# Kernel tuning notes

Measured on AMD Instinct MI355X. Metric: run time of the kernel, lower is better.

## Reference

```python
import jax, jax.numpy as jnp
import numpy as np

N = 100000      # nodes
E = 1600000     # edges (before self loops)
G = 64          # graphs (drones)
H = 4           # heads
C = 64          # hidden_channels (per-head dim, concat=False)
NODE_F = 32
DRONE_F = 16
OUT = 32
L = 2           # num_layers
LN_EPS = 1e-5
NEG_SLOPE = 0.2


def setup_inputs() -> dict:
    key = jax.random.key(0)
    ks = jax.random.split(key, 20)
    gn = lambda k, shape, s=0.1: jax.random.normal(k, shape, jnp.float32) * s
    inp = {}
    inp["x"] = jax.random.normal(ks[0], (N, NODE_F), jnp.float32)
    inp["drone_feat"] = jax.random.normal(ks[1], (G, DRONE_F), jnp.float32)
    inp["edge_index"] = jax.random.randint(ks[2], (2, E), 0, N, jnp.int32)
    inp["batch"] = jnp.sort(jax.random.randint(ks[3], (N,), 0, G, jnp.int32))
    inp["node_W"] = gn(ks[4], (C, NODE_F)); inp["node_b"] = jnp.zeros((C,), jnp.float32)
    inp["drone_W"] = gn(ks[5], (C, DRONE_F)); inp["drone_b"] = jnp.zeros((C,), jnp.float32)
    for l in range(L):
        kk = jax.random.split(ks[6 + l], 3)
        inp[f"convW{l}"] = gn(kk[0], (H * C, C))
        inp[f"att_src{l}"] = gn(kk[1], (H, C))
        inp[f"att_dst{l}"] = gn(kk[2], (H, C))
        inp[f"convb{l}"] = jnp.zeros((C,), jnp.float32)
        inp[f"ln_g{l}"] = jnp.ones((C,), jnp.float32)
        inp[f"ln_b{l}"] = jnp.zeros((C,), jnp.float32)
    inp["out_W"] = gn(ks[10], (OUT, C)); inp["out_b"] = jnp.zeros((OUT,), jnp.float32)
    return inp


def _layer_norm(x, g, b):
    mu = jnp.mean(x, axis=-1, keepdims=True)
    var = jnp.mean((x - mu) ** 2, axis=-1, keepdims=True)
    return (x - mu) * jax.lax.rsqrt(var + LN_EPS) * g + b


def _gat_conv(h, src, dst, W, a_src, a_dst, b):
    # h: [N, C] -> per-head transform [N, H, C]
    xh = (h @ W.T).reshape(N, H, C)
    alpha_s = jnp.sum(xh * a_src[None], axis=-1)  # [N, H]
    alpha_d = jnp.sum(xh * a_dst[None], axis=-1)  # [N, H]
    e = jax.nn.leaky_relu(alpha_s[src] + alpha_d[dst], NEG_SLOPE)  # [E', H]
    m = jax.ops.segment_max(e, dst, num_segments=N)  # segment softmax over dst
    ex = jnp.exp(e - m[dst])
    s = jax.ops.segment_sum(ex, dst, num_segments=N)
    alpha = ex / (s[dst] + 1e-16)                   # [E', H]
    out = jax.ops.segment_sum(xh[src] * alpha[:, :, None], dst, num_segments=N)
    return jnp.mean(out, axis=1) + b                # concat=False -> head mean


def reference(x, edge_index, drone_feat, batch, node_W, node_b, drone_W, drone_b,
              convW0, att_src0, att_dst0, convb0, ln_g0, ln_b0,
              convW1, att_src1, att_dst1, convb1, ln_g1, ln_b1,
              out_W, out_b):
    # add self loops (PyG GATConv default add_self_loops=True)
    loop = jnp.arange(N, dtype=edge_index.dtype)
    src = jnp.concatenate([edge_index[0], loop])
    dst = jnp.concatenate([edge_index[1], loop])
    h = x @ node_W.T + node_b + (drone_feat @ drone_W.T + drone_b)[batch]
    layers = [(convW0, att_src0, att_dst0, convb0, ln_g0, ln_b0),
              (convW1, att_src1, att_dst1, convb1, ln_g1, ln_b1)]
    for (W, a_s, a_d, cb, g, lb) in layers:
        h = h + jax.nn.relu(_layer_norm(_gat_conv(h, src, dst, W, a_s, a_d, cb), g, lb))
    return h @ out_W.T + out_b
```

## Files before the change

### kernel.cpp

```cpp
#include <hip/hip_runtime.h>
#include <hip/hip_fp16.h>
#include <math.h>


#define NEG_SLOPE 0.2f
#define LN_EPS 1e-5f

struct __align__(8) h16x4 { __half x, y, z, w; };

__global__ __launch_bounds__(256) void k_h0(
        const float* __restrict__ x, const int* __restrict__ batch,
        const float* __restrict__ node_W, const float* __restrict__ drone_W,
        const float* __restrict__ node_b, const float* __restrict__ drone_b,
        const float* __restrict__ drone_feat,
        float* __restrict__ h, int* __restrict__ cnt, int N) {
    __shared__ float xs[16][33];
    __shared__ float ds[16][17];
    __shared__ float wn[32][65];
    __shared__ float wd[16][65];
    __shared__ float bs[64];
    int t = threadIdx.x;
    int n0 = blockIdx.x * 16;
    for (int i = t; i < 2048; i += 256) { int co = i >> 5, k = i & 31; wn[k][co] = node_W[i]; }
    for (int i = t; i < 1024; i += 256) { int co = i >> 4, k = i & 15; wd[k][co] = drone_W[i]; }
    if (t < 64) bs[t] = node_b[t] + drone_b[t];
    for (int i = t; i < 512; i += 256) {
        int r = i >> 5, c = i & 31;
        int n = n0 + r;
        xs[r][c] = (n < N) ? x[(size_t)n * 32 + c] : 0.f;
    }
    {
        int r = t >> 4, c = t & 15;
        int n = n0 + r;
        int g = (n < N) ? batch[n] : 0;
        ds[r][c] = drone_feat[g * 16 + c];
    }
    {
        int gt = blockIdx.x * 256 + t;
        if (gt < N) cnt[gt] = 0;
    }
    __syncthreads();
    int co = t & 63;
    int nsub = t >> 6;
    float b = bs[co];
    float a0 = b, a1 = b, a2 = b, a3 = b;
#pragma unroll
    for (int k = 0; k < 32; ++k) {
        float w = wn[k][co];
        a0 = fmaf(xs[nsub * 4 + 0][k], w, a0);
        a1 = fmaf(xs[nsub * 4 + 1][k], w, a1);
        a2 = fmaf(xs[nsub * 4 + 2][k], w, a2);
        a3 = fmaf(xs[nsub * 4 + 3][k], w, a3);
    }
#pragma unroll
    for (int k = 0; k < 16; ++k) {
        float w = wd[k][co];
        a0 = fmaf(ds[nsub * 4 + 0][k], w, a0);
        a1 = fmaf(ds[nsub * 4 + 1][k], w, a1);
        a2 = fmaf(ds[nsub * 4 + 2][k], w, a2);
        a3 = fmaf(ds[nsub * 4 + 3][k], w, a3);
    }
    float av[4] = {a0, a1, a2, a3};
#pragma unroll
    for (int j = 0; j < 4; ++j) {
        int n = n0 + nsub * 4 + j;
        if (n < N) h[(size_t)n * 64 + co] = av[j];
    }
}

__global__ void k_scatter(const int* __restrict__ edge_index, int* __restrict__ cnt,
                          int* __restrict__ csrB,
                          const float* __restrict__ cW0, const float* __restrict__ cW1,
                          const float* __restrict__ s0, const float* __restrict__ d0,
                          const float* __restrict__ s1, const float* __restrict__ d1,
                          const float* __restrict__ out_W,
                          float* __restrict__ wt0, float* __restrict__ wt1,
                          float* __restrict__ uv, float* __restrict__ owT,
                          int E, int S) {
    if (blockIdx.y == 0 && blockIdx.x < 128) {
        int i = blockIdx.x * 256 + threadIdx.x;
        {
            int j = i & 16383;
            int co = j >> 6, k = j & 63;
            if (i < 16384) wt0[k * 256 + co] = cW0[j];
            else           wt1[k * 256 + co] = cW1[j];
        }
        if (i < 2048) {
            int k = i >> 5, o = i & 31;
            owT[i] = out_W[o * 64 + k];
        }
        if (i < 1024) {
            int l = i >> 9, sd = (i >> 8) & 1, head = (i >> 6) & 3, kk = i & 63;
            const float* W   = l ? cW1 : cW0;
            const float* att = l ? (sd ? d1 : s1) : (sd ? d0 : s0);
            float acc = 0.f;
            for (int c = 0; c < 64; ++c)
                acc += W[(head * 64 + c) * 64 + kk] * att[head * 64 + c];
            uv[i] = acc;
        }
    }
    int lo = blockIdx.y * S, hi = lo + S;
    int i = (blockIdx.x * blockDim.x + threadIdx.x) * 4;
    if (i + 3 < E) {
        int4 sv = *(const int4*)(edge_index + i);
        int4 dv = *(const int4*)(edge_index + E + i);
        int sl;
        if (dv.x >= lo && dv.x < hi) { sl = atomicAdd(cnt + dv.x, 1); if (sl < 63) csrB[((size_t)dv.x << 6) + 1 + sl] = sv.x; }
        if (dv.y >= lo && dv.y < hi) { sl = atomicAdd(cnt + dv.y, 1); if (sl < 63) csrB[((size_t)dv.y << 6) + 1 + sl] = sv.y; }
        if (dv.z >= lo && dv.z < hi) { sl = atomicAdd(cnt + dv.z, 1); if (sl < 63) csrB[((size_t)dv.z << 6) + 1 + sl] = sv.z; }
        if (dv.w >= lo && dv.w < hi) { sl = atomicAdd(cnt + dv.w, 1); if (sl < 63) csrB[((size_t)dv.w << 6) + 1 + sl] = sv.w; }
    } else {
        for (int k = i; k < E; ++k) {
            int d = edge_index[E + k];
            if (d >= lo && d < hi) {
                int sl = atomicAdd(cnt + d, 1);
                if (sl < 63) csrB[((size_t)d << 6) + 1 + sl] = edge_index[k];
            }
        }
    }
}

#define XPAD 68
__global__ __launch_bounds__(256) void k_xh(
        const float* __restrict__ h, const float* __restrict__ wt,
        const float* __restrict__ uv_l, __half* __restrict__ xh,
        float* __restrict__ as_, float* __restrict__ ad_, int N) {
    __shared__ float hs[32][XPAD];
    int t = threadIdx.x;
    int n0 = blockIdx.x * 32;
    for (int i = t; i < 32 * 64; i += 256) {
        int r = i >> 6, c = i & 63;
        int n = n0 + r;
        hs[r][c] = (n < N) ? h[(size_t)n * 64 + c] : 0.f;
    }
    __syncthreads();
    int co4 = (t & 63) * 4;
    int nsub = t >> 6;
    float4 acc[8];
#pragma unroll
    for (int j = 0; j < 8; ++j) acc[j] = make_float4(0.f, 0.f, 0.f, 0.f);
    const float* wp = wt + co4;
#pragma unroll 2
    for (int k4 = 0; k4 < 16; ++k4) {
        float4 w0 = *(const float4*)(wp + (k4 * 4 + 0) * 256);
        float4 w1 = *(const float4*)(wp + (k4 * 4 + 1) * 256);
        float4 w2 = *(const float4*)(wp + (k4 * 4 + 2) * 256);
        float4 w3 = *(const float4*)(wp + (k4 * 4 + 3) * 256);
#pragma unroll
        for (int j = 0; j < 8; ++j) {
            float4 hv = *(const float4*)&hs[nsub * 8 + j][k4 * 4];
            float4 a = acc[j];
            a.x = fmaf(hv.x, w0.x, fmaf(hv.y, w1.x, fmaf(hv.z, w2.x, fmaf(hv.w, w3.x, a.x))));
            a.y = fmaf(hv.x, w0.y, fmaf(hv.y, w1.y, fmaf(hv.z, w2.y, fmaf(hv.w, w3.y, a.y))));
            a.z = fmaf(hv.x, w0.z, fmaf(hv.y, w1.z, fmaf(hv.z, w2.z, fmaf(hv.w, w3.z, a.z))));
            a.w = fmaf(hv.x, w0.w, fmaf(hv.y, w1.w, fmaf(hv.z, w2.w, fmaf(hv.w, w3.w, a.w))));
            acc[j] = a;
        }
    }
#pragma unroll
    for (int j = 0; j < 8; ++j) {
        int n = n0 + nsub * 8 + j;
        if (n < N) {
            h16x4 o;
            o.x = __float2half(acc[j].x);
            o.y = __float2half(acc[j].y);
            o.z = __float2half(acc[j].z);
            o.w = __float2half(acc[j].w);
            *(h16x4*)(xh + (size_t)n * 256 + co4) = o;
        }
    }
    {
        int row  = t >> 3;
        int head = (t >> 1) & 3;
        int sd   = t & 1;
        int n = n0 + row;
        if (n < N) {
            const float* u = uv_l + sd * 256 + head * 64;
            float a = 0.f;
#pragma unroll
            for (int k4 = 0; k4 < 16; ++k4) {
                float4 hv = *(const float4*)&hs[row][k4 * 4];
                float4 uu = *(const float4*)(u + k4 * 4);
                a += hv.x * uu.x + hv.y * uu.y + hv.z * uu.z + hv.w * uu.w;
            }
            (sd ? ad_ : as_)[n * 4 + head] = a;
        }
    }
}

__device__ __forceinline__ __half2 shxor_h2(__half2 a, int m) {
    int u = __shfl_xor(*(int*)&a, m, 64);
    return *(__half2*)&u;
}

template <bool LAST>
__global__ __launch_bounds__(256) void k_gat(
        const __half* __restrict__ xh, const float* __restrict__ as_,
        const float* __restrict__ ad_, const int* __restrict__ cnt,
        const int* __restrict__ csrB, const float* __restrict__ convb,
        const float* __restrict__ ln_g, const float* __restrict__ ln_b,
        float* __restrict__ h, const float* __restrict__ owT,
        const float* __restrict__ out_b, float* __restrict__ out, int N) {
    __shared__ float owT_lds[2048];
    __shared__ float hout_lds4[4][64];
    int t = threadIdx.x;
    int wid = t >> 6, lane = t & 63;
    if (LAST) {
        for (int i = t; i < 2048; i += 256) owT_lds[i] = owT[i];
        __syncthreads();
    }
    int n = blockIdx.x * 4 + wid;
    if (n >= N) return;
    float* hout_lds = hout_lds4[wid];
    int g    = lane >> 4;
    int l16  = lane & 15;
    int head = l16 >> 2;
    int r0 = n << 6;
    int r1 = r0 + 1 + min(cnt[n], 63);
    float adv = ad_[(size_t)n * 4 + head];
    const __half* xb = xh + (size_t)l16 * 16;

    float s = 0.f;
    __half2 acc[8];
#pragma unroll
    for (int j = 0; j < 8; ++j) acc[j] = __float2half2_rn(0.f);

    uint4 zero4 = make_uint4(0u, 0u, 0u, 0u);
    int idx;
    idx = r0 + g;      bool vA = idx < r1; int sA = n; if (g != 0 && vA) sA = csrB[idx];
    idx = r0 + 4 + g;  bool vB = idx < r1; int sB = 0; if (vB) sB = csrB[idx];
    idx = r0 + 8 + g;  bool vC = idx < r1; int sC = 0; if (vC) sC = csrB[idx];
    idx = r0 + 12 + g; bool vD = idx < r1; int sD = 0; if (vD) sD = csrB[idx];
    float asA = 0.f, asB = 0.f;
    uint4 qA0 = zero4, qA1 = zero4, qB0 = zero4, qB1 = zero4;
    if (vA) {
        asA = as_[(size_t)sA * 4 + head];
        const uint4* bp = (const uint4*)(xb + (size_t)sA * 256);
        qA0 = bp[0]; qA1 = bp[1];
    }
    if (vB) {
        asB = as_[(size_t)sB * 4 + head];
        const uint4* bp = (const uint4*)(xb + (size_t)sB * 256);
        qB0 = bp[0]; qB1 = bp[1];
    }

    auto COMPUTE = [&](bool vc, float asc, const uint4& q0, const uint4& q1) {
        float e = asc + adv;
        e = e > 0.f ? e : NEG_SLOPE * e;
        float w = __expf(e);
        w = vc ? w : 0.f;
        s += w;
        __half2 w2 = __float2half2_rn(w);
        const __half2* ha = (const __half2*)&q0;
        const __half2* hb = (const __half2*)&q1;
        acc[0] = __hfma2(w2, ha[0], acc[0]);
        acc[1] = __hfma2(w2, ha[1], acc[1]);
        acc[2] = __hfma2(w2, ha[2], acc[2]);
        acc[3] = __hfma2(w2, ha[3], acc[3]);
        acc[4] = __hfma2(w2, hb[0], acc[4]);
        acc[5] = __hfma2(w2, hb[1], acc[5]);
        acc[6] = __hfma2(w2, hb[2], acc[6]);
        acc[7] = __hfma2(w2, hb[3], acc[7]);
    };

    for (int i = r0; i < r1; i += 8) {
        COMPUTE(vA, asA, qA0, qA1);
        int idxE = i + 16 + g; bool vE = idxE < r1; int sE = 0;
        if (vE) sE = csrB[idxE];
        vA = vC;
        if (vC) {
            asA = as_[(size_t)sC * 4 + head];
            const uint4* bp = (const uint4*)(xb + (size_t)sC * 256);
            qA0 = bp[0]; qA1 = bp[1];
        }
        COMPUTE(vB, asB, qB0, qB1);
        int idxF = i + 20 + g; bool vF = idxF < r1; int sF = 0;
        if (vF) sF = csrB[idxF];
        vB = vD;
        if (vD) {
            asB = as_[(size_t)sD * 4 + head];
            const uint4* bp = (const uint4*)(xb + (size_t)sD * 256);
            qB0 = bp[0]; qB1 = bp[1];
        }
        vC = vE; sC = sE;
        vD = vF; sD = sF;
    }

    s += __shfl_xor(s, 16, 64);
    s += __shfl_xor(s, 32, 64);
#pragma unroll
    for (int j = 0; j < 8; ++j) {
        acc[j] = __hadd2(acc[j], shxor_h2(acc[j], 16));
        acc[j] = __hadd2(acc[j], shxor_h2(acc[j], 32));
    }
    float inv = 1.f / (s + 1e-16f);
    float f[16];
#pragma unroll
    for (int j = 0; j < 8; ++j) {
        float2 tv = __half22float2(acc[j]);
        f[2 * j]     = tv.x * inv;
        f[2 * j + 1] = tv.y * inv;
    }
#pragma unroll
    for (int j = 0; j < 16; ++j) {
        f[j] += __shfl_xor(f[j], 4, 64);
        f[j] += __shfl_xor(f[j], 8, 64);
    }
    int cblk = lane & 3;
    int cb16 = cblk * 16;
    float o[16];
    float part = 0.f;
#pragma unroll
    for (int q = 0; q < 4; ++q) {
        float4 cb = *(const float4*)(convb + cb16 + q * 4);
        o[q * 4 + 0] = 0.25f * f[q * 4 + 0] + cb.x;
        o[q * 4 + 1] = 0.25f * f[q * 4 + 1] + cb.y;
        o[q * 4 + 2] = 0.25f * f[q * 4 + 2] + cb.z;
        o[q * 4 + 3] = 0.25f * f[q * 4 + 3] + cb.w;
        part += o[q * 4 + 0] + o[q * 4 + 1] + o[q * 4 + 2] + o[q * 4 + 3];
    }
    part += __shfl_xor(part, 1, 64);
    part += __shfl_xor(part, 2, 64);
    float mu = part * (1.f / 64.f);
    float vs = 0.f;
#pragma unroll
    for (int j = 0; j < 16; ++j) { o[j] -= mu; vs += o[j] * o[j]; }
    vs += __shfl_xor(vs, 1, 64);
    vs += __shfl_xor(vs, 2, 64);
    float rstd = rsqrtf(vs * (1.f / 64.f) + LN_EPS);

    if (!LAST) {
        if (lane < 4) {
            float4* hp = (float4*)(h + (size_t)n * 64 + cb16);
#pragma unroll
            for (int q = 0; q < 4; ++q) {
                float4 hv = hp[q];
                float4 gv = *(const float4*)(ln_g + cb16 + q * 4);
                float4 bv = *(const float4*)(ln_b + cb16 + q * 4);
                hv.x += fmaxf(o[q * 4 + 0] * rstd * gv.x + bv.x, 0.f);
                hv.y += fmaxf(o[q * 4 + 1] * rstd * gv.y + bv.y, 0.f);
                hv.z += fmaxf(o[q * 4 + 2] * rstd * gv.z + bv.z, 0.f);
                hv.w += fmaxf(o[q * 4 + 3] * rstd * gv.w + bv.w, 0.f);
                hp[q] = hv;
            }
        }
    } else {
        if (lane < 4) {
            const float4* hp = (const float4*)(h + (size_t)n * 64 + cb16);
#pragma unroll
            for (int q = 0; q < 4; ++q) {
                float4 hv = hp[q];
                float4 gv = *(const float4*)(ln_g + cb16 + q * 4);
                float4 bv = *(const float4*)(ln_b + cb16 + q * 4);
                hout_lds[cb16 + q * 4 + 0] = hv.x + fmaxf(o[q * 4 + 0] * rstd * gv.x + bv.x, 0.f);
                hout_lds[cb16 + q * 4 + 1] = hv.y + fmaxf(o[q * 4 + 1] * rstd * gv.y + bv.y, 0.f);
                hout_lds[cb16 + q * 4 + 2] = hv.z + fmaxf(o[q * 4 + 2] * rstd * gv.z + bv.z, 0.f);
                hout_lds[cb16 + q * 4 + 3] = hv.w + fmaxf(o[q * 4 + 3] * rstd * gv.w + bv.w, 0.f);
            }
        }
        asm volatile("s_waitcnt lgkmcnt(0)" ::: "memory");
        if (lane < 32) {
            float acc2 = out_b[lane];
#pragma unroll 8
            for (int k = 0; k < 64; ++k)
                acc2 = fmaf(hout_lds[k], owT_lds[k * 32 + lane], acc2);
            out[(size_t)n * 32 + lane] = acc2;
        }
    }
}

static inline unsigned cdiv(long long a, long long b) { return (unsigned)((a + b - 1) / b); }

extern "C" void kernel_launch(void* const* d_in, const int* in_sizes, int n_in,
                              void* d_out, int out_size, void* d_ws, size_t ws_size,
                              hipStream_t stream) {
    const float* x          = (const float*)d_in[0];
    const float* drone_feat = (const float*)d_in[1];
    const int*   edge_index = (const int*)d_in[2];
    const int*   batch      = (const int*)d_in[3];
    const float* node_W     = (const float*)d_in[4];
    const float* node_b     = (const float*)d_in[5];
    const float* drone_W    = (const float*)d_in[6];
    const float* drone_b    = (const float*)d_in[7];
    const float* convW[2]   = {(const float*)d_in[8],  (const float*)d_in[14]};
    const float* att_src[2] = {(const float*)d_in[9],  (const float*)d_in[15]};
    const float* att_dst[2] = {(const float*)d_in[10], (const float*)d_in[16]};
    const float* convb[2]   = {(const float*)d_in[11], (const float*)d_in[17]};
    const float* ln_g[2]    = {(const float*)d_in[12], (const float*)d_in[18]};
    const float* ln_b[2]    = {(const float*)d_in[13], (const float*)d_in[19]};
    const float* out_W      = (const float*)d_in[20];
    const float* out_b      = (const float*)d_in[21];
    float* out = (float*)d_out;

    const int N = in_sizes[0] / 32;
    const int E = in_sizes[2] / 2;
    const int P = 8;
    const int S = cdiv(N, P);

    char* base = (char*)d_ws;
    size_t off = 0;
    auto alloc = [&](size_t bytes) {
        char* p = base + off;
        off = (off + bytes + 255) & ~(size_t)255;
        return p;
    };
    float*           h      = (float*)alloc((size_t)N * 64 * 4);
    __half*          xh     = (__half*)alloc((size_t)N * 256 * 2);
    float*           as_    = (float*)alloc((size_t)N * 4 * 4);
    float*           ad_    = (float*)alloc((size_t)N * 4 * 4);
    float*           wt0    = (float*)alloc((size_t)256 * 64 * 4);
    float*           wt1    = (float*)alloc((size_t)256 * 64 * 4);
    float*           uv     = (float*)alloc((size_t)1024 * 4);
    float*           owT    = (float*)alloc((size_t)2048 * 4);
    int*             cnt    = (int*)alloc((size_t)N * 4);
    int*             csrB   = (int*)alloc((size_t)N * 64 * 4);
    (void)ws_size;
    const float* wt[2] = {wt0, wt1};

    k_h0<<<cdiv(N, 16), 256, 0, stream>>>(x, batch, node_W, drone_W, node_b, drone_b,
                                          drone_feat, h, cnt, N);
    {
        dim3 g(cdiv(cdiv(E, 4), 256), P);
        k_scatter<<<g, 256, 0, stream>>>(edge_index, cnt, csrB,
                                         convW[0], convW[1], att_src[0], att_dst[0],
                                         att_src[1], att_dst[1], out_W,
                                         wt0, wt1, uv, owT, E, S);
    }
    k_xh<<<cdiv(N, 32), 256, 0, stream>>>(h, wt[0], uv + 0 * 512, xh, as_, ad_, N);
    k_gat<false><<<cdiv(N, 4), 256, 0, stream>>>(xh, as_, ad_, cnt, csrB, convb[0],
                                                 ln_g[0], ln_b[0], h, owT, out_b, out, N);
    k_xh<<<cdiv(N, 32), 256, 0, stream>>>(h, wt[1], uv + 1 * 512, xh, as_, ad_, N);
    k_gat<true><<<cdiv(N, 4), 256, 0, stream>>>(xh, as_, ad_, cnt, csrB, convb[1],
                                                ln_g[1], ln_b[1], h, owT, out_b, out, N);
}
```

Measured before the change: 668.5 us.

## Drop partitioned scatter passes, use 32-bit offsets and half-precision reductions in GAT

The edge scatter no longer runs 8 destination-range partitions that each re-read the whole edge list. It now makes a single pass that issues atomics for every edge. In the GAT gather, 64-bit index arithmetic is replaced by unsigned 32-bit byte offsets, which cuts address computation. The normalization and cross-lane reductions now run on packed half2 values instead of 16 float shuffles, halving shuffle traffic at some cost in precision. The single-pass scatter trades the extra edge reads for scattered atomics with less locality.

```diff
diff --git a/kernel.cpp b/kernel.cpp
--- a/kernel.cpp
+++ b/kernel.cpp
@@ -76,8 +76,8 @@
                           const float* __restrict__ out_W,
                           float* __restrict__ wt0, float* __restrict__ wt1,
                           float* __restrict__ uv, float* __restrict__ owT,
-                          int E, int S) {
-    if (blockIdx.y == 0 && blockIdx.x < 128) {
+                          int E) {
+    if (blockIdx.x < 128) {
         int i = blockIdx.x * 256 + threadIdx.x;
         {
             int j = i & 16383;
@@ -99,23 +99,20 @@
             uv[i] = acc;
         }
     }
-    int lo = blockIdx.y * S, hi = lo + S;
     int i = (blockIdx.x * blockDim.x + threadIdx.x) * 4;
     if (i + 3 < E) {
         int4 sv = *(const int4*)(edge_index + i);
         int4 dv = *(const int4*)(edge_index + E + i);
         int sl;
-        if (dv.x >= lo && dv.x < hi) { sl = atomicAdd(cnt + dv.x, 1); if (sl < 63) csrB[((size_t)dv.x << 6) + 1 + sl] = sv.x; }
-        if (dv.y >= lo && dv.y < hi) { sl = atomicAdd(cnt + dv.y, 1); if (sl < 63) csrB[((size_t)dv.y << 6) + 1 + sl] = sv.y; }
-        if (dv.z >= lo && dv.z < hi) { sl = atomicAdd(cnt + dv.z, 1); if (sl < 63) csrB[((size_t)dv.z << 6) + 1 + sl] = sv.z; }
-        if (dv.w >= lo && dv.w < hi) { sl = atomicAdd(cnt + dv.w, 1); if (sl < 63) csrB[((size_t)dv.w << 6) + 1 + sl] = sv.w; }
+        sl = atomicAdd(cnt + dv.x, 1); if (sl < 63) csrB[((size_t)dv.x << 6) + 1 + sl] = sv.x;
+        sl = atomicAdd(cnt + dv.y, 1); if (sl < 63) csrB[((size_t)dv.y << 6) + 1 + sl] = sv.y;
+        sl = atomicAdd(cnt + dv.z, 1); if (sl < 63) csrB[((size_t)dv.z << 6) + 1 + sl] = sv.z;
+        sl = atomicAdd(cnt + dv.w, 1); if (sl < 63) csrB[((size_t)dv.w << 6) + 1 + sl] = sv.w;
     } else {
         for (int k = i; k < E; ++k) {
             int d = edge_index[E + k];
-            if (d >= lo && d < hi) {
-                int sl = atomicAdd(cnt + d, 1);
-                if (sl < 63) csrB[((size_t)d << 6) + 1 + sl] = edge_index[k];
-            }
+            int sl = atomicAdd(cnt + d, 1);
+            if (sl < 63) csrB[((size_t)d << 6) + 1 + sl] = edge_index[k];
         }
     }
 }
@@ -218,7 +215,9 @@
     int r0 = n << 6;
     int r1 = r0 + 1 + min(cnt[n], 63);
     float adv = ad_[(size_t)n * 4 + head];
-    const __half* xb = xh + (size_t)l16 * 16;
+    const char* xbb = (const char*)xh + (l16 << 5);
+    const char* asb = (const char*)as_ + (head << 2);
+    const char* cbb = (const char*)csrB;
 
     float s = 0.f;
     __half2 acc[8];
@@ -227,20 +226,20 @@
 
     uint4 zero4 = make_uint4(0u, 0u, 0u, 0u);
     int idx;
-    idx = r0 + g;      bool vA = idx < r1; int sA = n; if (g != 0 && vA) sA = csrB[idx];
-    idx = r0 + 4 + g;  bool vB = idx < r1; int sB = 0; if (vB) sB = csrB[idx];
-    idx = r0 + 8 + g;  bool vC = idx < r1; int sC = 0; if (vC) sC = csrB[idx];
-    idx = r0 + 12 + g; bool vD = idx < r1; int sD = 0; if (vD) sD = csrB[idx];
+    idx = r0 + g;      bool vA = idx < r1; int sA = n; if (g != 0 && vA) sA = *(const int*)(cbb + ((unsigned)idx << 2));
+    idx = r0 + 4 + g;  bool vB = idx < r1; int sB = 0; if (vB) sB = *(const int*)(cbb + ((unsigned)idx << 2));
+    idx = r0 + 8 + g;  bool vC = idx < r1; int sC = 0; if (vC) sC = *(const int*)(cbb + ((unsigned)idx << 2));
+    idx = r0 + 12 + g; bool vD = idx < r1; int sD = 0; if (vD) sD = *(const int*)(cbb + ((unsigned)idx << 2));
     float asA = 0.f, asB = 0.f;
     uint4 qA0 = zero4, qA1 = zero4, qB0 = zero4, qB1 = zero4;
     if (vA) {
-        asA = as_[(size_t)sA * 4 + head];
-        const uint4* bp = (const uint4*)(xb + (size_t)sA * 256);
+        asA = *(const float*)(asb + ((unsigned)sA << 4));
+        const uint4* bp = (const uint4*)(xbb + ((unsigned)sA << 9));
         qA0 = bp[0]; qA1 = bp[1];
     }
     if (vB) {
-        asB = as_[(size_t)sB * 4 + head];
-        const uint4* bp = (const uint4*)(xb + (size_t)sB * 256);
+        asB = *(const float*)(asb + ((unsigned)sB << 4));
+        const uint4* bp = (const uint4*)(xbb + ((unsigned)sB << 9));
         qB0 = bp[0]; qB1 = bp[1];
     }
 
@@ -266,20 +265,20 @@
     for (int i = r0; i < r1; i += 8) {
         COMPUTE(vA, asA, qA0, qA1);
         int idxE = i + 16 + g; bool vE = idxE < r1; int sE = 0;
-        if (vE) sE = csrB[idxE];
+        if (vE) sE = *(const int*)(cbb + ((unsigned)idxE << 2));
         vA = vC;
         if (vC) {
-            asA = as_[(size_t)sC * 4 + head];
-            const uint4* bp = (const uint4*)(xb + (size_t)sC * 256);
+            asA = *(const float*)(asb + ((unsigned)sC << 4));
+            const uint4* bp = (const uint4*)(xbb + ((unsigned)sC << 9));
             qA0 = bp[0]; qA1 = bp[1];
         }
         COMPUTE(vB, asB, qB0, qB1);
         int idxF = i + 20 + g; bool vF = idxF < r1; int sF = 0;
-        if (vF) sF = csrB[idxF];
+        if (vF) sF = *(const int*)(cbb + ((unsigned)idxF << 2));
         vB = vD;
         if (vD) {
-            asB = as_[(size_t)sD * 4 + head];
-            const uint4* bp = (const uint4*)(xb + (size_t)sD * 256);
+            asB = *(const float*)(asb + ((unsigned)sD << 4));
+            const uint4* bp = (const uint4*)(xbb + ((unsigned)sD << 9));
             qB0 = bp[0]; qB1 = bp[1];
         }
         vC = vE; sC = sE;
@@ -294,17 +293,19 @@
         acc[j] = __hadd2(acc[j], shxor_h2(acc[j], 32));
     }
     float inv = 1.f / (s + 1e-16f);
+    __half2 ih = __float2half2_rn(inv);
+#pragma unroll
+    for (int j = 0; j < 8; ++j) {
+        acc[j] = __hmul2(acc[j], ih);
+        acc[j] = __hadd2(acc[j], shxor_h2(acc[j], 4));
+        acc[j] = __hadd2(acc[j], shxor_h2(acc[j], 8));
+    }
     float f[16];
 #pragma unroll
     for (int j = 0; j < 8; ++j) {
         float2 tv = __half22float2(acc[j]);
-        f[2 * j]     = tv.x * inv;
-        f[2 * j + 1] = tv.y * inv;
-    }
-#pragma unroll
-    for (int j = 0; j < 16; ++j) {
-        f[j] += __shfl_xor(f[j], 4, 64);
-        f[j] += __shfl_xor(f[j], 8, 64);
+        f[2 * j]     = tv.x;
+        f[2 * j + 1] = tv.y;
     }
     int cblk = lane & 3;
     int cb16 = cblk * 16;
@@ -394,8 +395,6 @@
 
     const int N = in_sizes[0] / 32;
     const int E = in_sizes[2] / 2;
-    const int P = 8;
-    const int S = cdiv(N, P);
 
     char* base = (char*)d_ws;
     size_t off = 0;
@@ -419,13 +418,11 @@
 
     k_h0<<<cdiv(N, 16), 256, 0, stream>>>(x, batch, node_W, drone_W, node_b, drone_b,
                                           drone_feat, h, cnt, N);
-    {
-        dim3 g(cdiv(cdiv(E, 4), 256), P);
-        k_scatter<<<g, 256, 0, stream>>>(edge_index, cnt, csrB,
-                                         convW[0], convW[1], att_src[0], att_dst[0],
-                                         att_src[1], att_dst[1], out_W,
-                                         wt0, wt1, uv, owT, E, S);
-    }
+    k_scatter<<<cdiv(cdiv(E, 4), 256), 256, 0, stream>>>(
+        edge_index, cnt, csrB,
+        convW[0], convW[1], att_src[0], att_dst[0],
+        att_src[1], att_dst[1], out_W,
+        wt0, wt1, uv, owT, E);
     k_xh<<<cdiv(N, 32), 256, 0, stream>>>(h, wt[0], uv + 0 * 512, xh, as_, ad_, N);
     k_gat<false><<<cdiv(N, 4), 256, 0, stream>>>(xh, as_, ad_, cnt, csrB, convb[0],
                                                  ln_g[0], ln_b[0], h, owT, out_b, out, N);
```

Measured after the change: 727.2 us. +8.8%, slower.
